# Kernel optimization log

Hardware: AMD Instinct MI355X
Metric: run time of the kernel (lower is better)

## Reference

```python
import jax, jax.numpy as jnp
import numpy as np

B, T, C, H = 2, 2048, 1024, 16
SCALE = 0.02

def setup_inputs() -> dict:
    key = jax.random.key(0)
    ks = jax.random.split(key, 6)
    x = jax.random.normal(ks[0], (B, T, C), dtype=jnp.float32)
    Wq = jax.random.normal(ks[1], (C, C), dtype=jnp.float32) * SCALE
    Wk = jax.random.normal(ks[2], (C, C), dtype=jnp.float32) * SCALE
    Wv = jax.random.normal(ks[3], (C, C), dtype=jnp.float32) * SCALE
    Wp = jax.random.normal(ks[4], (C, C), dtype=jnp.float32) * SCALE
    z = jnp.zeros((C,), dtype=jnp.float32)
    return {"x": x, "Wq": Wq, "bq": z, "Wk": Wk, "bk": z, "Wv": Wv, "bv": z, "Wp": Wp, "bp": z}

def reference(x, Wq, bq, Wk, bk, Wv, bv, Wp, bp):
    b, t, c = x.shape
    hd = c // H  # head dim
    def split_heads(y):
        return y.reshape(b, t, H, hd).transpose(0, 2, 1, 3)  # [b,h,t,hd]
    q = split_heads(x @ Wq + bq)
    k = split_heads(x @ Wk + bk)
    v = split_heads(x @ Wv + bv)
    # explicit [b,h,t,t] scores with causal mask (tril), scaled by 1/sqrt(hd)
    att = jnp.einsum('bhqd,bhkd->bhqk', q, k) * (1.0 / jnp.sqrt(jnp.asarray(hd, x.dtype)))
    causal = jnp.tril(jnp.ones((t, t), dtype=bool))
    att = jnp.where(causal[None, None], att, jnp.asarray(-jnp.inf, att.dtype))
    att = jax.nn.softmax(att, axis=-1)
    y = jnp.einsum('bhqk,bhkd->bhqd', att, v)  # [b,h,t,hd]
    y = y.transpose(0, 2, 1, 3).reshape(b, t, c)
    return y @ Wp + bp
```

## Files before the change

### kernel.cpp

```cpp
#include <hip/hip_runtime.h>

typedef unsigned short u16;
typedef short s16x8 __attribute__((ext_vector_type(8)));
typedef unsigned short u16x4 __attribute__((ext_vector_type(4)));
typedef float f32x4 __attribute__((ext_vector_type(4)));

#define Bdim 2
#define Tdim 2048
#define Cdim 1024
#define Hn   16
#define HD   64
#define Mdim (Bdim*Tdim)

static __device__ __forceinline__ unsigned cvt_pk(float lo, float hi) {
  unsigned r;
  asm("v_cvt_pk_bf16_f32 %0, %1, %2" : "=v"(r) : "v"(lo), "v"(hi));
  return r;
}

static __device__ __forceinline__ void gload_lds16(const void* g, void* l) {
  __builtin_amdgcn_global_load_lds((const __attribute__((address_space(1))) void*)g,
                                   (__attribute__((address_space(3))) void*)l, 16, 0, 0);
}

__global__ __launch_bounds__(256) void cast_x_kernel(const float* __restrict__ in,
                                                     u16* __restrict__ out) {
  int i = (blockIdx.x * 256 + threadIdx.x) * 4;
  float4 f = *reinterpret_cast<const float4*>(in + i);
  uint2 o;
  o.x = cvt_pk(f.x, f.y);
  o.y = cvt_pk(f.z, f.w);
  *reinterpret_cast<uint2*>(out + i) = o;
}

__global__ __launch_bounds__(256) void transW_kernel(const float* __restrict__ Wq,
                                                     const float* __restrict__ Wk,
                                                     const float* __restrict__ Wv,
                                                     const float* __restrict__ Wp,
                                                     u16* __restrict__ Wt3,
                                                     u16* __restrict__ Wpt) {
  __shared__ u16 tile[64][72];
  const int z = blockIdx.z;
  const float* W = (z == 0) ? Wq : (z == 1) ? Wk : (z == 2) ? Wv : Wp;
  u16* dst = (z < 3) ? (Wt3 + (size_t)z * Cdim * Cdim) : Wpt;
  const int k0 = blockIdx.y * 64, n0 = blockIdx.x * 64;
  const int tx = threadIdx.x & 15, ty = threadIdx.x >> 4;
#pragma unroll
  for (int p = 0; p < 4; ++p) {
    float4 f = *reinterpret_cast<const float4*>(
        &W[(size_t)(k0 + ty + p * 16) * Cdim + n0 + tx * 4]);
    uint2 o;
    o.x = cvt_pk(f.x, f.y);
    o.y = cvt_pk(f.z, f.w);
    *reinterpret_cast<uint2*>(&tile[ty + p * 16][tx * 4]) = o;
  }
  __syncthreads();
#pragma unroll
  for (int p = 0; p < 4; ++p) {
    const int r = ty + p * 16;
    u16x4 w;
#pragma unroll
    for (int jj = 0; jj < 4; ++jj) w[jj] = tile[tx * 4 + jj][r];
    *reinterpret_cast<u16x4*>(&dst[(size_t)(n0 + r) * Cdim + k0 + tx * 4]) = w;
  }
}

template <int MODE, int BM, int BN>
__global__ __launch_bounds__(256) void gemm_bf16(
    const u16* __restrict__ A, const u16* __restrict__ Bt,
    const float* __restrict__ b0, const float* __restrict__ b1,
    const float* __restrict__ b2,
    u16* __restrict__ q_out, u16* __restrict__ k_out, u16* __restrict__ v_out,
    float* __restrict__ c_out) {
  constexpr int WM = BM / 2, WN = BN / 2, MI = WM / 16, NI = WN / 16;
  __shared__ __attribute__((aligned(16))) u16 As[BM * 32];
  __shared__ __attribute__((aligned(16))) u16 Bs[BN * 32];
  const int tid = threadIdx.x;
  const int lane = tid & 63, wave = tid >> 6;
  const int m0 = blockIdx.y * BM, n0 = blockIdx.x * BN;
  const int wm = (wave >> 1) * WM, wn = (wave & 1) * WN;
  const int lr = lane & 15, lk = (lane >> 4) * 8;
  const int srow = lane >> 2, scol = (lane & 3) * 8;
  f32x4 acc[MI][NI] = {};
  for (int k0 = 0; k0 < Cdim; k0 += 32) {
    __syncthreads();
#pragma unroll
    for (int i = 0; i < BM / 64; ++i) {
      const int slot = wave * (BM / 64) + i;
      const int row = slot * 16 + srow;
      gload_lds16(&A[(size_t)(m0 + row) * Cdim + k0 + scol], (char*)As + slot * 1024);
    }
#pragma unroll
    for (int i = 0; i < BN / 64; ++i) {
      const int slot = wave * (BN / 64) + i;
      const int row = slot * 16 + srow;
      gload_lds16(&Bt[(size_t)(n0 + row) * Cdim + k0 + scol], (char*)Bs + slot * 1024);
    }
    __syncthreads();
    s16x8 af[MI], bf[NI];
#pragma unroll
    for (int i = 0; i < MI; ++i)
      af[i] = *reinterpret_cast<const s16x8*>(&As[(wm + i * 16 + lr) * 32 + lk]);
#pragma unroll
    for (int i = 0; i < NI; ++i)
      bf[i] = *reinterpret_cast<const s16x8*>(&Bs[(wn + i * 16 + lr) * 32 + lk]);
#pragma unroll
    for (int mi = 0; mi < MI; ++mi)
#pragma unroll
      for (int ni = 0; ni < NI; ++ni)
        acc[mi][ni] = __builtin_amdgcn_mfma_f32_16x16x32_bf16(af[mi], bf[ni], acc[mi][ni], 0, 0, 0);
  }
  const int lc = lane & 15, lr4 = (lane >> 4) * 4;
  if (MODE == 0) {
    const int seg = n0 >> 10;
    const float* bias = (seg == 0) ? b0 : (seg == 1) ? b1 : b2;
    const int nb = n0 & 1023;
    if (seg < 2) {
      u16* dst = (seg == 0) ? q_out : k_out;
#pragma unroll
      for (int mi = 0; mi < MI; ++mi)
#pragma unroll
        for (int ni = 0; ni < NI; ++ni) {
          int mb = m0 + wm + mi * 16 + lr4;
          int n = nb + wn + ni * 16 + lc;
          float bn = bias[n];
          unsigned p01 = cvt_pk(acc[mi][ni][0] + bn, acc[mi][ni][1] + bn);
          unsigned p23 = cvt_pk(acc[mi][ni][2] + bn, acc[mi][ni][3] + bn);
          int b = mb >> 11, t = mb & 2047, h = n >> 6, d = n & 63;
          size_t base = (((size_t)(b * Hn + h)) * Tdim + t) * HD + d;
          dst[base]       = (u16)p01;
          dst[base + 64]  = (u16)(p01 >> 16);
          dst[base + 128] = (u16)p23;
          dst[base + 192] = (u16)(p23 >> 16);
        }
    } else {
#pragma unroll
      for (int mi = 0; mi < MI; ++mi)
#pragma unroll
        for (int ni = 0; ni < NI; ++ni) {
          int mbase = m0 + wm + mi * 16 + lr4;
          int n = nb + wn + ni * 16 + lc;
          float bn = bias[n];
          uint2 w;
          w.x = cvt_pk(acc[mi][ni][0] + bn, acc[mi][ni][1] + bn);
          w.y = cvt_pk(acc[mi][ni][2] + bn, acc[mi][ni][3] + bn);
          int b = mbase >> 11, t = mbase & 2047, h = n >> 6, d = n & 63;
          *reinterpret_cast<uint2*>(
              &v_out[(((size_t)(b * Hn + h)) * HD + d) * Tdim + t]) = w;
        }
    }
  } else {
#pragma unroll
    for (int mi = 0; mi < MI; ++mi)
#pragma unroll
      for (int ni = 0; ni < NI; ++ni)
#pragma unroll
        for (int j = 0; j < 4; ++j) {
          int m = m0 + wm + mi * 16 + lr4 + j;
          int n = n0 + wn + ni * 16 + lc;
          c_out[(size_t)m * Cdim + n] = acc[mi][ni][j] + b0[n];
        }
  }
}

__global__ __launch_bounds__(256) void attn_kernel(const u16* __restrict__ Qh,
                                                   const u16* __restrict__ Kh,
                                                   const u16* __restrict__ Vt,
                                                   u16* __restrict__ Yb) {
  __shared__ __attribute__((aligned(16))) u16 Ks[2][64 * 64];
  __shared__ __attribute__((aligned(16))) u16 Vs[2][64 * 64];
  __shared__ __attribute__((aligned(16))) u16 Ps[4][16 * 64];
  const int id = blockIdx.x;
  const int bh = id & 31;
  const int qblk = 31 - (id >> 5);
  const int tid = threadIdx.x;
  const int wave = tid >> 6, lane = tid & 63;
  const int lr = lane & 15, lg = lane >> 4;
  const int r0 = qblk * 64 + wave * 16;
  const int q_idx = r0 + lr;
  const u16* Qb = Qh + (size_t)bh * Tdim * HD;
  const u16* Kb = Kh + (size_t)bh * Tdim * HD;
  const u16* Vb = Vt + (size_t)bh * HD * Tdim;
  const float SC = 0.18033688011112042f;

  const int c1 = tid + 256;
  const int kr0 = tid >> 3, kc0 = (tid & 7) * 8, kw0 = kr0 * 64 + (kc0 ^ ((kr0 & 7) * 8));
  const int kr1 = c1 >> 3, kc1 = (c1 & 7) * 8, kw1 = kr1 * 64 + (kc1 ^ ((kr1 & 7) * 8));

  s16x8 bQ[2];
#pragma unroll
  for (int ks = 0; ks < 2; ++ks)
    bQ[ks] = *reinterpret_cast<const s16x8*>(&Qb[(size_t)q_idx * HD + ks * 32 + lg * 8]);

  float m = -1e30f, l = 0.f;
  f32x4 o[4];
#pragma unroll
  for (int di = 0; di < 4; ++di) o[di] = (f32x4){0.f, 0.f, 0.f, 0.f};

  s16x8 kg0, kg1, vg0, vg1;
  {
    kg0 = *reinterpret_cast<const s16x8*>(&Kb[(size_t)kr0 * HD + kc0]);
    kg1 = *reinterpret_cast<const s16x8*>(&Kb[(size_t)kr1 * HD + kc1]);
    vg0 = *reinterpret_cast<const s16x8*>(&Vb[(size_t)kr0 * Tdim + kc0]);
    vg1 = *reinterpret_cast<const s16x8*>(&Vb[(size_t)kr1 * Tdim + kc1]);
    *reinterpret_cast<s16x8*>(&Ks[0][kw0]) = kg0;
    *reinterpret_cast<s16x8*>(&Ks[0][kw1]) = kg1;
    *reinterpret_cast<s16x8*>(&Vs[0][kw0]) = vg0;
    *reinterpret_cast<s16x8*>(&Vs[0][kw1]) = vg1;
  }
  __syncthreads();

  const int swl = (lr & 7) * 8;
  for (int kb = 0; kb <= qblk; ++kb) {
    const int cur = kb & 1;
    if (kb < qblk) {
      const int kn = (kb + 1) * 64;
      kg0 = *reinterpret_cast<const s16x8*>(&Kb[(size_t)(kn + kr0) * HD + kc0]);
      kg1 = *reinterpret_cast<const s16x8*>(&Kb[(size_t)(kn + kr1) * HD + kc1]);
      vg0 = *reinterpret_cast<const s16x8*>(&Vb[(size_t)kr0 * Tdim + kn + kc0]);
      vg1 = *reinterpret_cast<const s16x8*>(&Vb[(size_t)kr1 * Tdim + kn + kc1]);
    }
    const int k0 = kb * 64;
    f32x4 st[4] = {};
    __builtin_amdgcn_s_setprio(1);
#pragma unroll
    for (int ni = 0; ni < 4; ++ni)
#pragma unroll
      for (int ks = 0; ks < 2; ++ks) {
        s16x8 aK = *reinterpret_cast<const s16x8*>(
            &Ks[cur][(ni * 16 + lr) * 64 + ((ks * 32 + lg * 8) ^ swl)]);
        st[ni] = __builtin_amdgcn_mfma_f32_16x16x32_bf16(aK, bQ[ks], st[ni], 0, 0, 0);
      }
    __builtin_amdgcn_s_setprio(0);
    if (kb == qblk) {
#pragma unroll
      for (int ni = 0; ni < 4; ++ni)
#pragma unroll
        for (int j = 0; j < 4; ++j)
          if (k0 + ni * 16 + lg * 4 + j > q_idx) st[ni][j] = -1e30f;
    }
    float t4[4];
#pragma unroll
    for (int ni = 0; ni < 4; ++ni)
      t4[ni] = fmaxf(fmaxf(st[ni][0], st[ni][1]), fmaxf(st[ni][2], st[ni][3]));
    float tm = fmaxf(fmaxf(t4[0], t4[1]), fmaxf(t4[2], t4[3]));
    tm = fmaxf(tm, __shfl_xor(tm, 16));
    tm = fmaxf(tm, __shfl_xor(tm, 32));
    const float tms = tm * SC;
    if (!__all(tms <= m + 8.0f)) {
      const float mn = fmaxf(m, tms);
      const float corr = exp2f(m - mn);
      l *= corr;
#pragma unroll
      for (int di = 0; di < 4; ++di)
#pragma unroll
        for (int j = 0; j < 4; ++j) o[di][j] *= corr;
      m = mn;
    }
    float rs = 0.f;
#pragma unroll
    for (int ni = 0; ni < 4; ++ni) {
      float p0 = exp2f(fmaf(st[ni][0], SC, -m));
      float p1 = exp2f(fmaf(st[ni][1], SC, -m));
      float p2 = exp2f(fmaf(st[ni][2], SC, -m));
      float p3 = exp2f(fmaf(st[ni][3], SC, -m));
      st[ni][0] = p0; st[ni][1] = p1; st[ni][2] = p2; st[ni][3] = p3;
      rs += (p0 + p1) + (p2 + p3);
    }
    rs += __shfl_xor(rs, 16);
    rs += __shfl_xor(rs, 32);
    l += rs;
#pragma unroll
    for (int ni = 0; ni < 4; ++ni) {
      uint2 pw;
      pw.x = cvt_pk(st[ni][0], st[ni][1]);
      pw.y = cvt_pk(st[ni][2], st[ni][3]);
      *reinterpret_cast<uint2*>(&Ps[wave][lr * 64 + ((ni * 16 + lg * 4) ^ swl)]) = pw;
    }
    s16x8 bP[2];
#pragma unroll
    for (int ks = 0; ks < 2; ++ks)
      bP[ks] = *reinterpret_cast<const s16x8*>(
          &Ps[wave][lr * 64 + ((ks * 32 + lg * 8) ^ swl)]);
    __builtin_amdgcn_s_setprio(1);
#pragma unroll
    for (int di = 0; di < 4; ++di)
#pragma unroll
      for (int ks = 0; ks < 2; ++ks) {
        s16x8 aV = *reinterpret_cast<const s16x8*>(
            &Vs[cur][(di * 16 + lr) * 64 + ((ks * 32 + lg * 8) ^ swl)]);
        o[di] = __builtin_amdgcn_mfma_f32_16x16x32_bf16(aV, bP[ks], o[di], 0, 0, 0);
      }
    __builtin_amdgcn_s_setprio(0);
    if (kb < qblk) {
      const int nxt = cur ^ 1;
      *reinterpret_cast<s16x8*>(&Ks[nxt][kw0]) = kg0;
      *reinterpret_cast<s16x8*>(&Ks[nxt][kw1]) = kg1;
      *reinterpret_cast<s16x8*>(&Vs[nxt][kw0]) = vg0;
      *reinterpret_cast<s16x8*>(&Vs[nxt][kw1]) = vg1;
    }
    __syncthreads();
  }
  const int b = bh >> 4, h = bh & 15;
  const float rl = 1.0f / l;
#pragma unroll
  for (int di = 0; di < 4; ++di) {
    uint2 w;
    w.x = cvt_pk(o[di][0] * rl, o[di][1] * rl);
    w.y = cvt_pk(o[di][2] * rl, o[di][3] * rl);
    *reinterpret_cast<uint2*>(
        &Yb[((size_t)(b * Tdim + q_idx)) * Cdim + h * 64 + di * 16 + lg * 4]) = w;
  }
}

extern "C" void kernel_launch(void* const* d_in, const int* in_sizes, int n_in,
                              void* d_out, int out_size, void* d_ws, size_t ws_size,
                              hipStream_t stream) {
  const float* x  = (const float*)d_in[0];
  const float* Wq = (const float*)d_in[1];
  const float* bq = (const float*)d_in[2];
  const float* Wk = (const float*)d_in[3];
  const float* bk = (const float*)d_in[4];
  const float* Wv = (const float*)d_in[5];
  const float* bv = (const float*)d_in[6];
  const float* Wp = (const float*)d_in[7];
  const float* bp = (const float*)d_in[8];
  float* out = (float*)d_out;
  char* ws = (char*)d_ws;

  u16* xb  = (u16*)(ws);
  u16* Wt3 = (u16*)(ws + ((size_t)8  << 20));
  u16* Wpt = (u16*)(ws + ((size_t)14 << 20));
  u16* Qh  = (u16*)(ws + ((size_t)16 << 20));
  u16* Kh  = (u16*)(ws + ((size_t)24 << 20));
  u16* Vt  = (u16*)(ws + ((size_t)32 << 20));
  u16* Yb  = (u16*)(ws + ((size_t)48 << 20));

  cast_x_kernel<<<4096, 256, 0, stream>>>(x, xb);
  transW_kernel<<<dim3(16, 16, 4), 256, 0, stream>>>(Wq, Wk, Wv, Wp, Wt3, Wpt);
  gemm_bf16<0, 128, 128><<<dim3(24, 32), 256, 0, stream>>>(xb, Wt3, bq, bk, bv,
                                                           Qh, Kh, Vt, nullptr);
  attn_kernel<<<1024, 256, 0, stream>>>(Qh, Kh, Vt, Yb);
  gemm_bf16<1, 64, 64><<<dim3(16, 64), 256, 0, stream>>>(Yb, Wpt, bp, nullptr, nullptr,
                                                         nullptr, nullptr, nullptr, out);
}
```

Measured before the change: 206.0 us.

## Deepen GEMM K-tile to 64 with XOR-swizzled LDS and XCD-aware block remap

The bf16 GEMM now stages 64-wide K slices instead of 32, which halves the number of barrier-separated iterations. Column chunks in LDS are XOR-swizzled by row to avoid bank conflicts on the fragment reads. Workgroup IDs are remapped so consecutive tiles land on the same XCD, improving L2 locality. The output projection also switches from 64x64 to 128x64 tiles. This doubles LDS use per block, which may reduce occupancy.

```diff
diff --git a/kernel.cpp b/kernel.cpp
--- a/kernel.cpp
+++ b/kernel.cpp
@@ -73,42 +73,57 @@
     u16* __restrict__ q_out, u16* __restrict__ k_out, u16* __restrict__ v_out,
     float* __restrict__ c_out) {
   constexpr int WM = BM / 2, WN = BN / 2, MI = WM / 16, NI = WN / 16;
-  __shared__ __attribute__((aligned(16))) u16 As[BM * 32];
-  __shared__ __attribute__((aligned(16))) u16 Bs[BN * 32];
+  __shared__ __attribute__((aligned(16))) u16 As[BM * 64];
+  __shared__ __attribute__((aligned(16))) u16 Bs[BN * 64];
   const int tid = threadIdx.x;
   const int lane = tid & 63, wave = tid >> 6;
-  const int m0 = blockIdx.y * BM, n0 = blockIdx.x * BN;
+  const int nwg = gridDim.x * gridDim.y;
+  const int id0 = blockIdx.y * gridDim.x + blockIdx.x;
+  const int q8 = nwg >> 3;
+  const int sid = (id0 & 7) * q8 + (id0 >> 3);
+  const int m0 = (sid / gridDim.x) * BM, n0 = (sid % gridDim.x) * BN;
   const int wm = (wave >> 1) * WM, wn = (wave & 1) * WN;
-  const int lr = lane & 15, lk = (lane >> 4) * 8;
-  const int srow = lane >> 2, scol = (lane & 3) * 8;
+  const int lr = lane & 15, lk4 = lane >> 4;
+  const int srow = lane >> 3;
+  const int scol = ((lane & 7) ^ srow) * 8;
   f32x4 acc[MI][NI] = {};
-  for (int k0 = 0; k0 < Cdim; k0 += 32) {
+  for (int k0 = 0; k0 < Cdim; k0 += 64) {
     __syncthreads();
 #pragma unroll
-    for (int i = 0; i < BM / 64; ++i) {
-      const int slot = wave * (BM / 64) + i;
-      const int row = slot * 16 + srow;
+    for (int i = 0; i < BM / 32; ++i) {
+      const int slot = wave * (BM / 32) + i;
+      const int row = slot * 8 + srow;
       gload_lds16(&A[(size_t)(m0 + row) * Cdim + k0 + scol], (char*)As + slot * 1024);
     }
 #pragma unroll
-    for (int i = 0; i < BN / 64; ++i) {
-      const int slot = wave * (BN / 64) + i;
-      const int row = slot * 16 + srow;
+    for (int i = 0; i < BN / 32; ++i) {
+      const int slot = wave * (BN / 32) + i;
+      const int row = slot * 8 + srow;
       gload_lds16(&Bt[(size_t)(n0 + row) * Cdim + k0 + scol], (char*)Bs + slot * 1024);
     }
     __syncthreads();
-    s16x8 af[MI], bf[NI];
-#pragma unroll
-    for (int i = 0; i < MI; ++i)
-      af[i] = *reinterpret_cast<const s16x8*>(&As[(wm + i * 16 + lr) * 32 + lk]);
-#pragma unroll
-    for (int i = 0; i < NI; ++i)
-      bf[i] = *reinterpret_cast<const s16x8*>(&Bs[(wn + i * 16 + lr) * 32 + lk]);
-#pragma unroll
-    for (int mi = 0; mi < MI; ++mi)
-#pragma unroll
-      for (int ni = 0; ni < NI; ++ni)
-        acc[mi][ni] = __builtin_amdgcn_mfma_f32_16x16x32_bf16(af[mi], bf[ni], acc[mi][ni], 0, 0, 0);
+#pragma unroll
+    for (int kk = 0; kk < 2; ++kk) {
+      s16x8 af[MI], bf[NI];
+#pragma unroll
+      for (int i = 0; i < MI; ++i) {
+        const int row = wm + i * 16 + lr;
+        af[i] = *reinterpret_cast<const s16x8*>(
+            &As[row * 64 + (((kk * 4 + lk4) ^ (lr & 7)) * 8)]);
+      }
+#pragma unroll
+      for (int i = 0; i < NI; ++i) {
+        const int row = wn + i * 16 + lr;
+        bf[i] = *reinterpret_cast<const s16x8*>(
+            &Bs[row * 64 + (((kk * 4 + lk4) ^ (lr & 7)) * 8)]);
+      }
+#pragma unroll
+      for (int mi = 0; mi < MI; ++mi)
+#pragma unroll
+        for (int ni = 0; ni < NI; ++ni)
+          acc[mi][ni] =
+              __builtin_amdgcn_mfma_f32_16x16x32_bf16(af[mi], bf[ni], acc[mi][ni], 0, 0, 0);
+    }
   }
   const int lc = lane & 15, lr4 = (lane >> 4) * 4;
   if (MODE == 0) {
@@ -341,6 +356,6 @@
   gemm_bf16<0, 128, 128><<<dim3(24, 32), 256, 0, stream>>>(xb, Wt3, bq, bk, bv,
                                                            Qh, Kh, Vt, nullptr);
   attn_kernel<<<1024, 256, 0, stream>>>(Qh, Kh, Vt, Yb);
-  gemm_bf16<1, 64, 64><<<dim3(16, 64), 256, 0, stream>>>(Yb, Wpt, bp, nullptr, nullptr,
-                                                         nullptr, nullptr, nullptr, out);
-}
+  gemm_bf16<1, 128, 64><<<dim3(16, 32), 256, 0, stream>>>(Yb, Wpt, bp, nullptr, nullptr,
+                                                          nullptr, nullptr, nullptr, out);
+}
```

New measurement: 198.6 us. 1.04x faster.
